# Kernel tuning notes

Measured on AMD Instinct MI355X. Metric: run time of the kernel, lower is better.

The kernel has to match this reference:

```python
import jax, jax.numpy as jnp
import numpy as np
import math

B, S, HID = 2, 2048, 1024
NUM_HEADS = 16
HEAD_DIM = HID // NUM_HEADS
SPARSITY_RATIO = 0.1
NEG = -1e9


def _make_sparse_mask(key, seq_len, sparsity_ratio):
    # local window: min(32, seq_len // 4), rows attend to |i - j| <= window // 2
    local_window = min(32, seq_len // 4)
    half = local_window // 2
    idx = jnp.arange(seq_len)
    mask = jnp.abs(idx[:, None] - idx[None, :]) <= half  # [S, S] bool
    # random global connections: n_global random columns per row
    n_global = int(seq_len * sparsity_ratio)
    gidx = jax.random.randint(key, (seq_len, n_global), 0, seq_len)
    mask = mask.at[idx[:, None], gidx].set(True)
    return mask


def setup_inputs() -> dict:
    key = jax.random.key(0)
    ks = jax.random.split(key, 6)
    lim = math.sqrt(6.0 / (HID + HID))  # xavier uniform bound
    def w(k):
        return jax.random.uniform(k, (HID, HID), jnp.float32, -lim, lim)
    return {
        "hidden_states": jax.random.normal(ks[0], (B, S, HID), jnp.float32),
        "Wq": w(ks[1]), "bq": jnp.zeros((HID,), jnp.float32),
        "Wk": w(ks[2]), "bk": jnp.zeros((HID,), jnp.float32),
        "Wv": w(ks[3]), "bv": jnp.zeros((HID,), jnp.float32),
        "Wo": w(ks[4]), "bo": jnp.zeros((HID,), jnp.float32),
        "sparse_mask": _make_sparse_mask(ks[5], S, SPARSITY_RATIO),
    }


def reference(hidden_states, Wq, bq, Wk, bk, Wv, bv, Wo, bo, sparse_mask):
    Bsz, seq, hid = hidden_states.shape
    H, D = NUM_HEADS, hid // NUM_HEADS

    def proj(W, b):
        y = hidden_states @ W.T + b                      # [B, S, hid]
        return y.reshape(Bsz, seq, H, D).transpose(0, 2, 1, 3)  # [B, H, S, D]

    q = proj(Wq, bq)
    k = proj(Wk, bk)
    v = proj(Wv, bv)

    scores = jnp.einsum("bhqd,bhkd->bhqk", q, k) / jnp.sqrt(jnp.float32(D))
    scores = jnp.where(sparse_mask[None, None, :, :], scores, jnp.float32(NEG))
    probs = jax.nn.softmax(scores, axis=-1)
    ctx = jnp.einsum("bhqk,bhkd->bhqd", probs, v)        # [B, H, S, D]
    ctx = ctx.transpose(0, 2, 1, 3).reshape(Bsz, seq, hid)
    return ctx @ Wo.T + bo
```

## Files before the change

kernel.cpp:

```cpp
#include <hip/hip_runtime.h>

typedef short bf16x8 __attribute__((ext_vector_type(8)));
typedef float f32x4 __attribute__((ext_vector_type(4)));
typedef unsigned short us4 __attribute__((ext_vector_type(4)));

#define S_LEN 2048
#define HIDD 1024
#define NH 16
#define HD 64

#define BK 64

static __device__ __forceinline__ unsigned short f2bf(float f) {
  union { float f; unsigned u; } v; v.f = f;
  unsigned r = v.u + 0x7FFFu + ((v.u >> 16) & 1u);
  return (unsigned short)(r >> 16);
}

static __device__ __forceinline__ unsigned cvtpk(float lo, float hi) {
  unsigned r;
  asm("v_cvt_pk_bf16_f32 %0, %1, %2" : "=v"(r) : "v"(lo), "v"(hi));
  return r;
}

static __device__ __forceinline__ float ex2(float x) {
#if __has_builtin(__builtin_amdgcn_exp2f)
  return __builtin_amdgcn_exp2f(x);
#else
  return __expf(x * 0.69314718056f);
#endif
}

#define GLD16(gp, lp)                                                        \
  __builtin_amdgcn_global_load_lds(                                         \
      (const __attribute__((address_space(1))) void*)(gp),                  \
      (__attribute__((address_space(3))) void*)(lp), 16, 0, 0)

__global__ __launch_bounds__(256) void cvt5_kernel(
    const float* __restrict__ s0, const float* __restrict__ s1, const float* __restrict__ s2,
    const float* __restrict__ s3, const float* __restrict__ s4,
    unsigned short* __restrict__ d0, unsigned short* __restrict__ d1,
    unsigned short* __restrict__ d2, unsigned short* __restrict__ d3,
    unsigned short* __restrict__ d4) {
  const float* s; unsigned short* d; int n4;
  switch (blockIdx.y) {
    case 0: s = s0; d = d0; n4 = (2 * S_LEN * HIDD) / 4; break;
    case 1: s = s1; d = d1; n4 = (HIDD * HIDD) / 4; break;
    case 2: s = s2; d = d2; n4 = (HIDD * HIDD) / 4; break;
    case 3: s = s3; d = d3; n4 = (HIDD * HIDD) / 4; break;
    default: s = s4; d = d4; n4 = (HIDD * HIDD) / 4; break;
  }
  for (int i = blockIdx.x * blockDim.x + threadIdx.x; i < n4;
       i += gridDim.x * blockDim.x) {
    float4 v = ((const float4*)s)[i];
    us4 o;
    o.x = f2bf(v.x); o.y = f2bf(v.y); o.z = f2bf(v.z); o.w = f2bf(v.w);
    ((us4*)d)[i] = o;
  }
}

__global__ __launch_bounds__(256) void maskbits_kernel(
    const unsigned char* __restrict__ m8, unsigned* __restrict__ bits) {
  int idx = blockIdx.x * 256 + threadIdx.x;
  int q = idx >> 6, w = idx & 63;
  bool bytemode = (m8[1] != 0);
  unsigned r = 0;
  if (bytemode) {
    const uint4* p = (const uint4*)(m8 + (size_t)q * 2048 + w * 32);
    uint4 a = p[0], b = p[1];
    unsigned v[8] = {a.x, a.y, a.z, a.w, b.x, b.y, b.z, b.w};
#pragma unroll
    for (int j = 0; j < 8; ++j)
#pragma unroll
      for (int k = 0; k < 4; ++k)
        r |= (((v[j] >> (k * 8)) & 255u) ? 1u : 0u) << (j * 4 + k);
  } else {
    const int4* p = (const int4*)((const int*)m8 + (size_t)q * 2048 + (size_t)w * 32);
#pragma unroll
    for (int j = 0; j < 8; ++j) {
      int4 v = p[j];
      r |= (v.x ? 1u : 0u) << (j * 4 + 0);
      r |= (v.y ? 1u : 0u) << (j * 4 + 1);
      r |= (v.z ? 1u : 0u) << (j * 4 + 2);
      r |= (v.w ? 1u : 0u) << (j * 4 + 3);
    }
  }
  bits[idx] = r;
}

template <int MFRAG>
static __device__ __forceinline__ void gemm_core2(
    const unsigned short* __restrict__ A, const unsigned short* __restrict__ W,
    int bm0, int bn0, unsigned short* As, unsigned short* Bs,
    f32x4 (&acc)[MFRAG][4]) {
  const int tid = threadIdx.x;
  const int lane = tid & 63;
  const int wid = tid >> 6;
  const int wr = wid >> 1, wc = wid & 1;
  const int l15 = lane & 15, g = lane >> 4, l7 = l15 & 7;
  const int ra = (g ^ l7) * 8;

  for (int k0 = 0; k0 < HIDD; k0 += BK) {
    __syncthreads();
#pragma unroll
    for (int it = 0; it < MFRAG; ++it) {
      int p = it * 256 + tid;
      int r = p >> 3, ch = (p & 7) ^ (r & 7);
      GLD16(A + (size_t)(bm0 + r) * HIDD + k0 + ch * 8,
            As + (it * 256 + wid * 64) * 8);
    }
#pragma unroll
    for (int it = 0; it < 4; ++it) {
      int p = it * 256 + tid;
      int r = p >> 3, ch = (p & 7) ^ (r & 7);
      GLD16(W + (size_t)(bn0 + r) * HIDD + k0 + ch * 8,
            Bs + (it * 256 + wid * 64) * 8);
    }
    __syncthreads();
#pragma unroll
    for (int kk = 0; kk < 2; ++kk) {
      bf16x8 af[MFRAG], bfr[4];
#pragma unroll
      for (int m = 0; m < MFRAG; ++m)
        af[m] = *(const bf16x8*)&As[(wr * (MFRAG * 16) + m * 16 + l15) * 64 + (ra ^ (kk * 32))];
#pragma unroll
      for (int n = 0; n < 4; ++n)
        bfr[n] = *(const bf16x8*)&Bs[(wc * 64 + n * 16 + l15) * 64 + (ra ^ (kk * 32))];
#pragma unroll
      for (int m = 0; m < MFRAG; ++m)
#pragma unroll
        for (int n = 0; n < 4; ++n)
          acc[m][n] = __builtin_amdgcn_mfma_f32_16x16x32_bf16(af[m], bfr[n], acc[m][n], 0, 0, 0);
    }
  }
}

__global__ __launch_bounds__(256) void gemm_qkv(
    const unsigned short* __restrict__ hs,
    const unsigned short* __restrict__ Wq, const unsigned short* __restrict__ Wk,
    const unsigned short* __restrict__ Wv,
    const float* __restrict__ bq, const float* __restrict__ bk, const float* __restrict__ bv,
    unsigned short* __restrict__ Qs, unsigned short* __restrict__ Kb,
    unsigned short* __restrict__ VT) {
  __shared__ __align__(16) unsigned short As[128 * 64];
  __shared__ __align__(16) unsigned short Bs[128 * 64];
  const int z = blockIdx.z;
  const unsigned short* W = (z == 0) ? Wq : ((z == 1) ? Wk : Wv);
  const float* bias = (z == 0) ? bq : ((z == 1) ? bk : bv);

  f32x4 acc[4][4];
#pragma unroll
  for (int m = 0; m < 4; ++m)
#pragma unroll
    for (int n = 0; n < 4; ++n) acc[m][n] = (f32x4){0.f, 0.f, 0.f, 0.f};

  const int bm0 = blockIdx.x * 128, bn0 = blockIdx.y * 128;
  gemm_core2<4>(hs, W, bm0, bn0, As, Bs, acc);

  const int lane = threadIdx.x & 63;
  const int wid = threadIdx.x >> 6;
  const int wr = wid >> 1, wc = wid & 1;
  const int l15 = lane & 15, g = lane >> 4;
  const float qscale = 0.125f * 1.44269504088896f;

#pragma unroll
  for (int m = 0; m < 4; ++m) {
#pragma unroll
    for (int n = 0; n < 4; ++n) {
      int grow0 = bm0 + wr * 64 + m * 16 + g * 4;
      int gcol = bn0 + wc * 64 + n * 16 + l15;
      float bv_ = bias[gcol];
      if (z == 0) {
#pragma unroll
        for (int i = 0; i < 4; ++i)
          Qs[(size_t)(grow0 + i) * HIDD + gcol] = f2bf((acc[m][n][i] + bv_) * qscale);
      } else if (z == 1) {
#pragma unroll
        for (int i = 0; i < 4; ++i)
          Kb[(size_t)(grow0 + i) * HIDD + gcol] = f2bf(acc[m][n][i] + bv_);
      } else {
        int b = grow0 >> 11, s = grow0 & 2047;
        int h = gcol >> 6, d = gcol & 63;
        us4 pk;
#pragma unroll
        for (int i = 0; i < 4; ++i) pk[i] = f2bf(acc[m][n][i] + bv_);
        *(us4*)&VT[((size_t)(b * NH + h) * HD + d) * S_LEN + s] = pk;
      }
    }
  }
}

__global__ __launch_bounds__(256) void gemm_o(
    const unsigned short* __restrict__ ctx, const unsigned short* __restrict__ Wo,
    const float* __restrict__ bo, float* __restrict__ out) {
  __shared__ __align__(16) unsigned short As[64 * 64];
  __shared__ __align__(16) unsigned short Bs[128 * 64];
  f32x4 acc[2][4];
#pragma unroll
  for (int m = 0; m < 2; ++m)
#pragma unroll
    for (int n = 0; n < 4; ++n) acc[m][n] = (f32x4){0.f, 0.f, 0.f, 0.f};

  const int bm0 = blockIdx.x * 64, bn0 = blockIdx.y * 128;
  gemm_core2<2>(ctx, Wo, bm0, bn0, As, Bs, acc);

  const int lane = threadIdx.x & 63;
  const int wid = threadIdx.x >> 6;
  const int wr = wid >> 1, wc = wid & 1;
  const int l15 = lane & 15, g = lane >> 4;
#pragma unroll
  for (int m = 0; m < 2; ++m) {
#pragma unroll
    for (int n = 0; n < 4; ++n) {
      int grow0 = bm0 + wr * 32 + m * 16 + g * 4;
      int gcol = bn0 + wc * 64 + n * 16 + l15;
      float bv_ = bo[gcol];
#pragma unroll
      for (int i = 0; i < 4; ++i)
        out[(size_t)(grow0 + i) * HIDD + gcol] = acc[m][n][i] + bv_;
    }
  }
}

__global__ __launch_bounds__(512) void attn4_kernel(
    const unsigned short* __restrict__ Qs, const unsigned short* __restrict__ Kb,
    const unsigned short* __restrict__ VT, const unsigned* __restrict__ mbits,
    unsigned short* __restrict__ ctx) {
  __shared__ __align__(16) unsigned short Kt[2][4096];
  __shared__ __align__(16) unsigned short Vt[2][4096];
  __shared__ __align__(16) unsigned short Pl[8][16][72];

  const int tid = threadIdx.x;
  const int wid = tid >> 6, lane = tid & 63;
  const int l15 = lane & 15, g = lane >> 4;
  const int l7 = l15 & 7;
  const int b = blockIdx.x >> 4, h = blockIdx.x & 15;
  const int qrow = blockIdx.y * 128 + wid * 16 + l15;

  const unsigned short* Kbh = Kb + (size_t)b * S_LEN * HIDD + h * HD;
  const unsigned short* VTbh = VT + (size_t)(b * NH + h) * HD * S_LEN;

  const unsigned short* Qrow = Qs + (size_t)(b * S_LEN + qrow) * HIDD + h * HD;
  bf16x8 qf0 = *(const bf16x8*)(Qrow + g * 8);
  bf16x8 qf1 = *(const bf16x8*)(Qrow + 32 + g * 8);

  const unsigned* mrow = mbits + (size_t)qrow * 64;

  const int rb0 = l15 * 64 + ((g ^ l7)) * 8;
  const int rb1 = l15 * 64 + ((g ^ l7) ^ 4) * 8;

  const bool isK = (wid < 4);
  const int wk = wid & 3;
  {
  }
  int p0 = wk * 128 + lane;
  int p1 = p0 + 64;
  int r0 = p0 >> 3, c0 = (p0 & 7) ^ (r0 & 7);
  int r1 = p1 >> 3, c1 = (p1 & 7) ^ (r1 & 7);
  const unsigned short* gp0;
  const unsigned short* gp1;
  int gstep;
  unsigned short* lp0;
  if (isK) {
    gp0 = Kbh + (size_t)r0 * HIDD + c0 * 8;
    gp1 = Kbh + (size_t)r1 * HIDD + c1 * 8;
    gstep = 64 * HIDD;
    lp0 = &Kt[0][0] + wk * 1024;
  } else {
    gp0 = VTbh + (size_t)r0 * S_LEN + c0 * 8;
    gp1 = VTbh + (size_t)r1 * S_LEN + c1 * 8;
    gstep = 64;
    lp0 = &Vt[0][0] + wk * 1024;
  }
  unsigned short* lp1 = lp0 + 512;

  float m_run = -1e8f, l_run = 0.f;
  f32x4 oacc[4];
#pragma unroll
  for (int dc = 0; dc < 4; ++dc) oacc[dc] = (f32x4){0.f, 0.f, 0.f, 0.f};

  GLD16(gp0, lp0);
  GLD16(gp1, lp1);
  gp0 += gstep; gp1 += gstep;
  uint2 mw = *(const uint2*)mrow;
  __syncthreads();

  for (int it = 0; it < 32; ++it) {
    const int tb = ((it + 1) & 1) * 4096;
    GLD16(gp0, lp0 + tb);
    GLD16(gp1, lp1 + tb);
    gp0 += gstep; gp1 += gstep;
    uint2 mw_n = *(const uint2*)(mrow + (it + 1) * 2);

    const unsigned short* Kbuf = &Kt[it & 1][0];
    f32x4 sacc[4];
#pragma unroll
    for (int t = 0; t < 4; ++t) {
      sacc[t] = (f32x4){0.f, 0.f, 0.f, 0.f};
      bf16x8 ka = *(const bf16x8*)(Kbuf + t * 1024 + rb0);
      bf16x8 kb2 = *(const bf16x8*)(Kbuf + t * 1024 + rb1);
      sacc[t] = __builtin_amdgcn_mfma_f32_16x16x32_bf16(ka, qf0, sacc[t], 0, 0, 0);
      sacc[t] = __builtin_amdgcn_mfma_f32_16x16x32_bf16(kb2, qf1, sacc[t], 0, 0, 0);
    }

    float t0 = fmaxf(fmaxf(sacc[0][0], sacc[0][1]), sacc[0][2]);
    float t1 = fmaxf(fmaxf(sacc[0][3], sacc[1][0]), sacc[1][1]);
    float t2 = fmaxf(fmaxf(sacc[1][2], sacc[1][3]), sacc[2][0]);
    float t3 = fmaxf(fmaxf(sacc[2][1], sacc[2][2]), sacc[2][3]);
    float t4 = fmaxf(fmaxf(sacc[3][0], sacc[3][1]), sacc[3][2]);
    float t5 = fmaxf(fmaxf(t0, t1), sacc[3][3]);
    float pmax = fmaxf(fmaxf(fmaxf(t2, t3), t4), t5);
    pmax = fmaxf(pmax, __shfl_xor(pmax, 16));
    pmax = fmaxf(pmax, __shfl_xor(pmax, 32));

    if (__any(pmax > m_run + 8.0f)) {
      float m_new = fmaxf(m_run, pmax);
      float corr = ex2(m_run - m_new);
      l_run *= corr;
#pragma unroll
      for (int dc = 0; dc < 4; ++dc) oacc[dc] *= corr;
      m_run = m_new;
    }

    float lsum = 0.f;
#pragma unroll
    for (int t = 0; t < 4; ++t) {
      unsigned word = (t & 2) ? mw.y : mw.x;
      unsigned nib = word >> ((t & 1) * 16 + g * 4);
      float e0 = ex2(sacc[t][0] - m_run);
      float e1 = ex2(sacc[t][1] - m_run);
      float e2 = ex2(sacc[t][2] - m_run);
      float e3 = ex2(sacc[t][3] - m_run);
      float q0 = (nib & 1u) ? e0 : 0.f;
      float q1 = (nib & 2u) ? e1 : 0.f;
      float q2 = (nib & 4u) ? e2 : 0.f;
      float q3 = (nib & 8u) ? e3 : 0.f;
      lsum += (q0 + q1) + (q2 + q3);
      uint2 w2;
      w2.x = cvtpk(q0, q1);
      w2.y = cvtpk(q2, q3);
      *(uint2*)&Pl[wid][l15][t * 16 + g * 4] = w2;
    }
    lsum += __shfl_xor(lsum, 16);
    lsum += __shfl_xor(lsum, 32);
    l_run += lsum;

    bf16x8 pf0 = *(const bf16x8*)&Pl[wid][l15][g * 8];
    bf16x8 pf1 = *(const bf16x8*)&Pl[wid][l15][32 + g * 8];

    const unsigned short* Vbuf = &Vt[it & 1][0];
#pragma unroll
    for (int dc = 0; dc < 4; ++dc) {
      bf16x8 va = *(const bf16x8*)(Vbuf + dc * 1024 + rb0);
      bf16x8 vb = *(const bf16x8*)(Vbuf + dc * 1024 + rb1);
      oacc[dc] = __builtin_amdgcn_mfma_f32_16x16x32_bf16(va, pf0, oacc[dc], 0, 0, 0);
      oacc[dc] = __builtin_amdgcn_mfma_f32_16x16x32_bf16(vb, pf1, oacc[dc], 0, 0, 0);
    }

    mw = mw_n;
    __syncthreads();
  }

  float inv_l = 1.f / l_run;
  unsigned short* crow = ctx + (size_t)(b * S_LEN + qrow) * HIDD + h * HD;
#pragma unroll
  for (int dc = 0; dc < 4; ++dc) {
    uint2 o;
    o.x = cvtpk(oacc[dc][0] * inv_l, oacc[dc][1] * inv_l);
    o.y = cvtpk(oacc[dc][2] * inv_l, oacc[dc][3] * inv_l);
    *(uint2*)&crow[dc * 16 + g * 4] = o;
  }
}

extern "C" void kernel_launch(void* const* d_in, const int* in_sizes, int n_in,
                              void* d_out, int out_size, void* d_ws, size_t ws_size,
                              hipStream_t stream) {
  const float* hs = (const float*)d_in[0];
  const float* Wq = (const float*)d_in[1];
  const float* bq = (const float*)d_in[2];
  const float* Wk = (const float*)d_in[3];
  const float* bk = (const float*)d_in[4];
  const float* Wv = (const float*)d_in[5];
  const float* bv = (const float*)d_in[6];
  const float* Wo = (const float*)d_in[7];
  const float* bo = (const float*)d_in[8];
  const unsigned char* mask = (const unsigned char*)d_in[9];

  char* ws = (char*)d_ws;
  unsigned short* hs_bf = (unsigned short*)(ws);
  unsigned short* Wq_bf = (unsigned short*)(ws + (8u << 20));
  unsigned short* Wk_bf = (unsigned short*)(ws + (10u << 20));
  unsigned short* Wv_bf = (unsigned short*)(ws + (12u << 20));
  unsigned short* Wo_bf = (unsigned short*)(ws + (14u << 20));
  unsigned short* Qs    = (unsigned short*)(ws + (16u << 20));
  unsigned short* Kbf   = (unsigned short*)(ws + (24u << 20));
  unsigned short* VT    = (unsigned short*)(ws + (32u << 20));
  unsigned short* ctxb  = (unsigned short*)(ws + (40u << 20));
  unsigned* mbits = (unsigned*)(ws);
  float* out = (float*)d_out;

  cvt5_kernel<<<dim3(256, 5), 256, 0, stream>>>(hs, Wq, Wk, Wv, Wo,
                                                hs_bf, Wq_bf, Wk_bf, Wv_bf, Wo_bf);
  gemm_qkv<<<dim3(32, 8, 3), 256, 0, stream>>>(hs_bf, Wq_bf, Wk_bf, Wv_bf,
                                               bq, bk, bv, Qs, Kbf, VT);
  maskbits_kernel<<<512, 256, 0, stream>>>(mask, mbits);
  attn4_kernel<<<dim3(32, 16), 512, 0, stream>>>(Qs, Kbf, VT, mbits, ctxb);
  gemm_o<<<dim3(64, 8), 256, 0, stream>>>(ctxb, Wo_bf, bo, out);
}
```

Baseline: 139.9 us.

## Split attention KV range across two blocks and merge with combine kernel

```diff
diff --git a/kernel.cpp b/kernel.cpp
--- a/kernel.cpp
+++ b/kernel.cpp
@@ -15,6 +15,11 @@
   union { float f; unsigned u; } v; v.f = f;
   unsigned r = v.u + 0x7FFFu + ((v.u >> 16) & 1u);
   return (unsigned short)(r >> 16);
+}
+
+static __device__ __forceinline__ float bf2f(unsigned short u) {
+  union { unsigned u; float f; } v; v.u = ((unsigned)u) << 16;
+  return v.f;
 }
 
 static __device__ __forceinline__ unsigned cvtpk(float lo, float hi) {
@@ -222,10 +227,11 @@
   }
 }
 
-__global__ __launch_bounds__(512) void attn4_kernel(
+__global__ __launch_bounds__(512) void attn5_kernel(
     const unsigned short* __restrict__ Qs, const unsigned short* __restrict__ Kb,
     const unsigned short* __restrict__ VT, const unsigned* __restrict__ mbits,
-    unsigned short* __restrict__ ctx) {
+    unsigned short* __restrict__ part0, unsigned short* __restrict__ part1,
+    float2* __restrict__ ml) {
   __shared__ __align__(16) unsigned short Kt[2][4096];
   __shared__ __align__(16) unsigned short Vt[2][4096];
   __shared__ __align__(16) unsigned short Pl[8][16][72];
@@ -235,6 +241,8 @@
   const int l15 = lane & 15, g = lane >> 4;
   const int l7 = l15 & 7;
   const int b = blockIdx.x >> 4, h = blockIdx.x & 15;
+  const int z = blockIdx.z;
+  const int kvbase = z * 1024;
   const int qrow = blockIdx.y * 128 + wid * 16 + l15;
 
   const unsigned short* Kbh = Kb + (size_t)b * S_LEN * HIDD + h * HD;
@@ -244,15 +252,13 @@
   bf16x8 qf0 = *(const bf16x8*)(Qrow + g * 8);
   bf16x8 qf1 = *(const bf16x8*)(Qrow + 32 + g * 8);
 
-  const unsigned* mrow = mbits + (size_t)qrow * 64;
+  const unsigned* mrow = mbits + (size_t)qrow * 64 + z * 32;
 
   const int rb0 = l15 * 64 + ((g ^ l7)) * 8;
   const int rb1 = l15 * 64 + ((g ^ l7) ^ 4) * 8;
 
   const bool isK = (wid < 4);
   const int wk = wid & 3;
-  {
-  }
   int p0 = wk * 128 + lane;
   int p1 = p0 + 64;
   int r0 = p0 >> 3, c0 = (p0 & 7) ^ (r0 & 7);
@@ -262,13 +268,13 @@
   int gstep;
   unsigned short* lp0;
   if (isK) {
-    gp0 = Kbh + (size_t)r0 * HIDD + c0 * 8;
-    gp1 = Kbh + (size_t)r1 * HIDD + c1 * 8;
+    gp0 = Kbh + (size_t)(kvbase + r0) * HIDD + c0 * 8;
+    gp1 = Kbh + (size_t)(kvbase + r1) * HIDD + c1 * 8;
     gstep = 64 * HIDD;
     lp0 = &Kt[0][0] + wk * 1024;
   } else {
-    gp0 = VTbh + (size_t)r0 * S_LEN + c0 * 8;
-    gp1 = VTbh + (size_t)r1 * S_LEN + c1 * 8;
+    gp0 = VTbh + (size_t)r0 * S_LEN + kvbase + c0 * 8;
+    gp1 = VTbh + (size_t)r1 * S_LEN + kvbase + c1 * 8;
     gstep = 64;
     lp0 = &Vt[0][0] + wk * 1024;
   }
@@ -285,7 +291,7 @@
   uint2 mw = *(const uint2*)mrow;
   __syncthreads();
 
-  for (int it = 0; it < 32; ++it) {
+  for (int it = 0; it < 16; ++it) {
     const int tb = ((it + 1) & 1) * 4096;
     GLD16(gp0, lp0 + tb);
     GLD16(gp1, lp1 + tb);
@@ -361,14 +367,51 @@
     __syncthreads();
   }
 
-  float inv_l = 1.f / l_run;
-  unsigned short* crow = ctx + (size_t)(b * S_LEN + qrow) * HIDD + h * HD;
+  float linv = 1.f / fmaxf(l_run, 1e-37f);
+  unsigned short* obase = (z == 0) ? part0 : part1;
+  unsigned short* crow = obase + (size_t)(b * S_LEN + qrow) * HIDD + h * HD;
 #pragma unroll
   for (int dc = 0; dc < 4; ++dc) {
     uint2 o;
-    o.x = cvtpk(oacc[dc][0] * inv_l, oacc[dc][1] * inv_l);
-    o.y = cvtpk(oacc[dc][2] * inv_l, oacc[dc][3] * inv_l);
+    o.x = cvtpk(oacc[dc][0] * linv, oacc[dc][1] * linv);
+    o.y = cvtpk(oacc[dc][2] * linv, oacc[dc][3] * linv);
     *(uint2*)&crow[dc * 16 + g * 4] = o;
+  }
+  if (g == 0) {
+    ml[(size_t)z * (32 * S_LEN) + (size_t)blockIdx.x * S_LEN + qrow] =
+        make_float2(m_run, l_run);
+  }
+}
+
+__global__ __launch_bounds__(256) void combine_kernel(
+    const unsigned short* p1, const float2* __restrict__ ml,
+    unsigned short* p0 ) {
+  int gid = blockIdx.x * 256 + threadIdx.x;
+  int r = gid >> 2;
+  int dq = (gid & 3) * 16;
+  float2 a = ml[r];
+  float2 c = ml[65536 + r];
+  float m = fmaxf(a.x, c.x);
+  float w0 = a.y * ex2(a.x - m);
+  float w1 = c.y * ex2(c.x - m);
+  float inv = 1.f / (w0 + w1);
+  w0 *= inv; w1 *= inv;
+  int bh = r >> 11, q = r & 2047;
+  int b = bh >> 4, h = bh & 15;
+  size_t off = ((size_t)(b * S_LEN + q)) * HIDD + h * HD + dq;
+#pragma unroll
+  for (int half = 0; half < 2; ++half) {
+    bf16x8 o0 = *(const bf16x8*)(p0 + off + half * 8);
+    bf16x8 o1 = *(const bf16x8*)(p1 + off + half * 8);
+    unsigned res[4];
+#pragma unroll
+    for (int j = 0; j < 4; ++j) {
+      float v0 = w0 * bf2f((unsigned short)o0[2 * j]) + w1 * bf2f((unsigned short)o1[2 * j]);
+      float v1 = w0 * bf2f((unsigned short)o0[2 * j + 1]) + w1 * bf2f((unsigned short)o1[2 * j + 1]);
+      res[j] = cvtpk(v0, v1);
+    }
+    uint4 st = {res[0], res[1], res[2], res[3]};
+    *(uint4*)(p0 + off + half * 8) = st;
   }
 }
 
@@ -396,7 +439,9 @@
   unsigned short* Kbf   = (unsigned short*)(ws + (24u << 20));
   unsigned short* VT    = (unsigned short*)(ws + (32u << 20));
   unsigned short* ctxb  = (unsigned short*)(ws + (40u << 20));
-  unsigned* mbits = (unsigned*)(ws);
+  unsigned* mbits       = (unsigned*)(ws);
+  unsigned short* part1 = (unsigned short*)(ws + (1u << 19));
+  float2* ml            = (float2*)(ws + (9u << 20));
   float* out = (float*)d_out;
 
   cvt5_kernel<<<dim3(256, 5), 256, 0, stream>>>(hs, Wq, Wk, Wv, Wo,
@@ -404,6 +449,8 @@
   gemm_qkv<<<dim3(32, 8, 3), 256, 0, stream>>>(hs_bf, Wq_bf, Wk_bf, Wv_bf,
                                                bq, bk, bv, Qs, Kbf, VT);
   maskbits_kernel<<<512, 256, 0, stream>>>(mask, mbits);
-  attn4_kernel<<<dim3(32, 16), 512, 0, stream>>>(Qs, Kbf, VT, mbits, ctxb);
+  attn5_kernel<<<dim3(32, 16, 2), 512, 0, stream>>>(Qs, Kbf, VT, mbits,
+                                                    ctxb, part1, ml);
+  combine_kernel<<<1024, 256, 0, stream>>>(part1, ml, ctxb);
   gemm_o<<<dim3(64, 8), 256, 0, stream>>>(ctxb, Wo_bf, bo, out);
 }
```

Result: slower. 146.9 us (+5.0%).
